# Performance work log

Measured on AMD Instinct MI355X. Metric: run time of the kernel, lower is better.

The kernel has to match this reference:

```python
import jax, jax.numpy as jnp
import numpy as np
import math

B, S, D, H = 2, 2048, 768, 12
HD = D // H


def setup_inputs() -> dict:
    key = jax.random.key(0)
    ks = jax.random.split(key, 9)
    scale = 1.0 / math.sqrt(D)
    x = jax.random.normal(ks[0], (B, S, D), dtype=jnp.float32)
    # causal mask: True where attention is allowed (query i attends to key j<=i)
    mask = jnp.tril(jnp.ones((S, S), dtype=bool))[None, None]  # [1,1,S,S]
    wq = jax.random.normal(ks[1], (D, D), dtype=jnp.float32) * scale
    bq = jnp.zeros((D,), dtype=jnp.float32)
    wk = jax.random.normal(ks[2], (D, D), dtype=jnp.float32) * scale
    bk = jnp.zeros((D,), dtype=jnp.float32)
    wv = jax.random.normal(ks[3], (D, D), dtype=jnp.float32) * scale
    bv = jnp.zeros((D,), dtype=jnp.float32)
    wo = jax.random.normal(ks[4], (D, D), dtype=jnp.float32) * scale
    bo = jnp.zeros((D,), dtype=jnp.float32)
    return {"x": x, "mask": mask, "wq": wq, "bq": bq, "wk": wk, "bk": bk,
            "wv": wv, "bv": bv, "wo": wo, "bo": bo}


def reference(x, mask, wq, bq, wk, bk, wv, bv, wo, bo):
    b, s, d = x.shape
    # projections (flax Linear: y = x @ kernel + bias)
    q = (x @ wq + bq).reshape(b, s, H, HD).transpose(0, 2, 1, 3)  # [b,h,s,hd]
    k = (x @ wk + bk).reshape(b, s, H, HD).transpose(0, 2, 1, 3)
    v = (x @ wv + bv).reshape(b, s, H, HD).transpose(0, 2, 1, 3)
    scores = jnp.einsum('bhqd,bhkd->bhqk', q, k) / math.sqrt(HD)  # [b,h,s,s]
    scores = jnp.where(mask, scores, -jnp.inf)
    attn = jax.nn.softmax(scores, axis=-1)
    out = jnp.einsum('bhqk,bhkd->bhqd', attn, v)  # [b,h,s,hd]
    out = out.transpose(0, 2, 1, 3).reshape(b, s, d)
    return out @ wo + bo
```

## Files before the change

kernel.cpp:

```cpp
#include <hip/hip_runtime.h>
#include <math.h>

#define BATCH 2
#define SEQ   2048
#define DMODEL 768
#define NHEAD 12
#define HDIM  64

typedef unsigned short u16;
typedef __attribute__((ext_vector_type(8))) short bf16x8;
typedef __attribute__((ext_vector_type(4))) float f32x4;
typedef __attribute__((ext_vector_type(8))) unsigned short us8;
typedef __attribute__((ext_vector_type(4))) unsigned short us4;

__device__ __forceinline__ u16 f2bf(float f) {
    union { float f; unsigned u; } v; v.f = f;
    unsigned u = v.u;
    u += 0x7fff + ((u >> 16) & 1);
    return (u16)(u >> 16);
}

__device__ __forceinline__ u16 f2bf_trunc(float f) {
    union { float f; unsigned u; } v; v.f = f;
    return (u16)(v.u >> 16);
}

__device__ __forceinline__ void g2l16(const void* g, void* l) {
    __builtin_amdgcn_global_load_lds(
        (const __attribute__((address_space(1))) unsigned int*)g,
        (__attribute__((address_space(3))) unsigned int*)(unsigned int)(unsigned long long)(uintptr_t)l,
        16, 0, 0);
}

__device__ __forceinline__ void stage_rows(const u16* g, u16* lds, int nrows,
                                           int tid) {
    const int row = tid >> 2, col = (tid & 3) * 8;
    g2l16(g + (size_t)row * DMODEL + col, lds + tid * 8);
    if (nrows == 128) {
        g2l16(g + (size_t)(row + 64) * DMODEL + col, lds + 2048 + tid * 8);
    } else if (nrows == 96) {
        if (tid < 128)
            g2l16(g + (size_t)(row + 64) * DMODEL + col, lds + 2048 + tid * 8);
    }
}

__global__ __launch_bounds__(256) void prep(const float* __restrict__ x,
                                            const float* __restrict__ w0,
                                            const float* __restrict__ w1,
                                            const float* __restrict__ w2,
                                            const float* __restrict__ w3,
                                            u16* __restrict__ xb,
                                            u16* __restrict__ Wt_all) {
    __shared__ float t[32][33];
    const int bid = blockIdx.x;
    if (bid < 3072) {
        int i = bid * 256 + threadIdx.x;
        float4 v = ((const float4*)x)[i];
        us4 o;
        o.x = f2bf(v.x); o.y = f2bf(v.y); o.z = f2bf(v.z); o.w = f2bf(v.w);
        *(us4*)&xb[(size_t)i * 4] = o;
    } else {
        const int wid = bid - 3072;
        const int z  = wid / 576;
        const int rr = wid % 576;
        const int by = rr / 24, bx = rr % 24;
        const float* W = z == 0 ? w0 : z == 1 ? w1 : z == 2 ? w2 : w3;
        u16* Wt = Wt_all + (size_t)z * DMODEL * DMODEL;

        int tx = threadIdx.x & 31, ty = threadIdx.x >> 5;
        int xg = bx * 32 + tx;
        #pragma unroll
        for (int j = 0; j < 32; j += 8)
            t[ty + j][tx] = W[(size_t)(by * 32 + ty + j) * DMODEL + xg];
        __syncthreads();
        int x2 = by * 32 + tx;
        #pragma unroll
        for (int j = 0; j < 32; j += 8)
            Wt[(size_t)(bx * 32 + ty + j) * DMODEL + x2] = f2bf(t[tx][ty + j]);
    }
}

__global__ __launch_bounds__(256) void gemm_qkv(
    const u16* __restrict__ xb, const u16* __restrict__ WtQK,
    const u16* __restrict__ WtV,
    const float* __restrict__ bq, const float* __restrict__ bk,
    const float* __restrict__ bv,
    u16* __restrict__ QK, u16* __restrict__ Vt) {

    __shared__ __align__(16) u16 As[128 * 32];
    __shared__ __align__(16) u16 Bs[128 * 32];

    const int tid  = threadIdx.x;
    const int lane = tid & 63;
    const int w    = tid >> 6;
    const int quad = lane >> 4, l16 = lane & 15;
    const int wm   = w >> 1, wn = w & 1;
    const int b    = blockIdx.x;

    if (b < 512) {
        const int m0 = (b >> 4) * 128;
        const int n0 = (b & 15) * 96;
        f32x4 acc[4][3] = {};
        for (int k0 = 0; k0 < DMODEL; k0 += 32) {
            stage_rows(xb   + (size_t)m0 * DMODEL + k0, As, 128, tid);
            stage_rows(WtQK + (size_t)n0 * DMODEL + k0, Bs,  96, tid);
            __syncthreads();
            bf16x8 af[4], bfr[3];
            #pragma unroll
            for (int i = 0; i < 4; ++i)
                af[i] = *(const bf16x8*)&As[(wm * 64 + i * 16 + l16) * 32 + quad * 8];
            #pragma unroll
            for (int j = 0; j < 3; ++j)
                bfr[j] = *(const bf16x8*)&Bs[(wn * 48 + j * 16 + l16) * 32 + quad * 8];
            #pragma unroll
            for (int i = 0; i < 4; ++i)
                #pragma unroll
                for (int j = 0; j < 3; ++j)
                    acc[i][j] = __builtin_amdgcn_mfma_f32_16x16x32_bf16(af[i], bfr[j], acc[i][j], 0, 0, 0);
            __syncthreads();
        }
        const size_t n_elem = (size_t)BATCH * SEQ * DMODEL;
        #pragma unroll
        for (int j = 0; j < 3; ++j) {
            const int n     = n0 + wn * 48 + j * 16 + l16;
            const int which = n / 768;
            const int nn    = n - which * 768;
            const float bias  = (which == 0 ? bq : bk)[nn];
            const float scale = (which == 0) ? 0.125f : 1.0f;
            const int h = nn >> 6, hd = nn & 63;
            u16* outw = QK + (size_t)which * n_elem;
            #pragma unroll
            for (int i = 0; i < 4; ++i) {
                const int mbase = m0 + wm * 64 + i * 16 + quad * 4;
                #pragma unroll
                for (int r = 0; r < 4; ++r) {
                    const int m  = mbase + r;
                    const int b_ = m >> 11, s_ = m & 2047;
                    outw[(size_t)((b_ * NHEAD + h) * SEQ + s_) * HDIM + hd] =
                        f2bf((acc[i][j][r] + bias) * scale);
                }
            }
        }
    } else {
        const int vj = b - 512;
        const int m0 = (vj & 7) * 96;
        const int n0 = (vj >> 3) * 128;
        f32x4 acc[3][4] = {};
        for (int k0 = 0; k0 < DMODEL; k0 += 32) {
            stage_rows(WtV + (size_t)m0 * DMODEL + k0, As,  96, tid);
            stage_rows(xb  + (size_t)n0 * DMODEL + k0, Bs, 128, tid);
            __syncthreads();
            bf16x8 af[3], bfr[4];
            #pragma unroll
            for (int i = 0; i < 3; ++i)
                af[i] = *(const bf16x8*)&As[(wm * 48 + i * 16 + l16) * 32 + quad * 8];
            #pragma unroll
            for (int j = 0; j < 4; ++j)
                bfr[j] = *(const bf16x8*)&Bs[(wn * 64 + j * 16 + l16) * 32 + quad * 8];
            #pragma unroll
            for (int i = 0; i < 3; ++i)
                #pragma unroll
                for (int j = 0; j < 4; ++j)
                    acc[i][j] = __builtin_amdgcn_mfma_f32_16x16x32_bf16(af[i], bfr[j], acc[i][j], 0, 0, 0);
            __syncthreads();
        }
        #pragma unroll
        for (int i = 0; i < 3; ++i) {
            const int rbase = m0 + wm * 48 + i * 16 + quad * 4;
            #pragma unroll
            for (int r = 0; r < 4; ++r) {
                const int row_g = rbase + r;
                const float bias = bv[row_g];
                const int h = row_g >> 6, hd = row_g & 63;
                #pragma unroll
                for (int j = 0; j < 4; ++j) {
                    const int col_g = n0 + wn * 64 + j * 16 + l16;
                    const int b_ = col_g >> 11, s_ = col_g & 2047;
                    Vt[(size_t)((b_ * NHEAD + h) * HDIM + hd) * SEQ + s_] =
                        f2bf(acc[i][j][r] + bias);
                }
            }
        }
    }
}

__global__ __launch_bounds__(256) void gemm_out(
    const u16* __restrict__ Ag, const u16* __restrict__ Bt,
    const float* __restrict__ bo, float* __restrict__ out) {

    __shared__ __align__(16) u16 As[64 * 32];
    __shared__ __align__(16) u16 Bs[64 * 32];

    const int tid  = threadIdx.x;
    const int lane = tid & 63;
    const int w    = tid >> 6;
    const int quad = lane >> 4, l16 = lane & 15;
    const int wm   = w >> 1, wn = w & 1;
    const int m0 = blockIdx.x * 64, n0 = blockIdx.y * 64;

    const int rowA = tid >> 2;
    const int kch  = (tid & 3) * 8;

    f32x4 acc[2][2] = {};

    for (int k0 = 0; k0 < DMODEL; k0 += 32) {
        g2l16(Ag + (size_t)(m0 + rowA) * DMODEL + k0 + kch, As + tid * 8);
        g2l16(Bt + (size_t)(n0 + rowA) * DMODEL + k0 + kch, Bs + tid * 8);
        __syncthreads();

        bf16x8 af[2], bfr[2];
        #pragma unroll
        for (int i = 0; i < 2; ++i)
            af[i] = *(const bf16x8*)&As[(wm * 32 + i * 16 + l16) * 32 + quad * 8];
        #pragma unroll
        for (int j = 0; j < 2; ++j)
            bfr[j] = *(const bf16x8*)&Bs[(wn * 32 + j * 16 + l16) * 32 + quad * 8];
        #pragma unroll
        for (int i = 0; i < 2; ++i)
            #pragma unroll
            for (int j = 0; j < 2; ++j)
                acc[i][j] = __builtin_amdgcn_mfma_f32_16x16x32_bf16(af[i], bfr[j], acc[i][j], 0, 0, 0);
        __syncthreads();
    }

    #pragma unroll
    for (int i = 0; i < 2; ++i) {
        const int mbase = m0 + wm * 32 + i * 16 + quad * 4;
        #pragma unroll
        for (int r = 0; r < 4; ++r) {
            const int m = mbase + r;
            #pragma unroll
            for (int j = 0; j < 2; ++j) {
                const int n = n0 + wn * 32 + j * 16 + l16;
                out[(size_t)m * DMODEL + n] = acc[i][j][r] + bo[n];
            }
        }
    }
}

__global__ __launch_bounds__(256) void flash_attn_mfma(
    const u16* __restrict__ Q, const u16* __restrict__ K,
    const u16* __restrict__ Vt, u16* __restrict__ A) {

    __shared__ __align__(16) u16 Kl[2][64 * 64];
    __shared__ __align__(16) u16 Vl[2][64 * 64];
    __shared__ __align__(16) u16 Pl[4][16 * 72];

    const int tid  = threadIdx.x;
    const int lane = tid & 63;
    const int w    = tid >> 6;
    const int quad = lane >> 4;
    const int l16  = lane & 15;

    const int lin = blockIdx.x;
    const int cc_ = lin & 255, rk = lin >> 8;
    const int sid = (rk << 8) + ((rk & 1) ? (255 - cc_) : cc_);
    const int j   = sid / 24;
    const int bh  = sid - j * 24;
    const int tc  = j + 1;

    const size_t base = (size_t)bh * SEQ * HDIM;
    const u16* Qg = Q + base;
    const u16* Kg = K + base;
    const u16* Vg = Vt + base;

    const int wrow0 = j * 64 + w * 16;
    const int qrow  = wrow0 + quad * 4;

    bf16x8 qf0 = *(const bf16x8*)&Qg[(size_t)(wrow0 + l16) * 64 + quad * 8];
    bf16x8 qf1 = *(const bf16x8*)&Qg[(size_t)(wrow0 + l16) * 64 + quad * 8 + 32];

    f32x4 o[4] = {};
    float l_acc[4] = {0.f, 0.f, 0.f, 0.f};

    const int pwbase = 2 * quad + (l16 >> 3);
    const int prd0   = (quad + 2 * (l16 >> 2)) & 7;
    u16* Pw = Pl[w];
    const u16* pr0 = &Pw[l16 * 72 + prd0 * 8];
    const u16* pr1 = &Pw[l16 * 72 + (prd0 ^ 4) * 8];

    auto STAGE = [&](int t, int b) {
        const int j0 = t * 64;
        #pragma unroll
        for (int h = 0; h < 2; ++h) {
            const int ch = tid + h * 256;
            const int r  = ch >> 3;
            const int lc = (ch & 7) ^ (r & 7);
            g2l16(Kg + (size_t)(j0 + r) * 64 + lc * 8, &Kl[b][ch * 8]);
            g2l16(Vg + (size_t)r * SEQ + j0 + lc * 8,  &Vl[b][ch * 8]);
        }
    };

    STAGE(0, 0);
    __syncthreads();

    int cur = 0;
    for (int t = 0; t < tc; ++t) {
        if (t + 1 < tc) STAGE(t + 1, cur ^ 1);

        const int j0 = t * 64;
        const u16* Kc = Kl[cur];
        const u16* Vc = Vl[cur];

        f32x4 s[4];
        #pragma unroll
        for (int c4 = 0; c4 < 4; ++c4) {
            const int krow = c4 * 16 + l16;
            const int pc = (quad ^ (krow & 7)) * 8;
            bf16x8 kf0 = *(const bf16x8*)&Kc[krow * 64 + pc];
            bf16x8 kf1 = *(const bf16x8*)&Kc[krow * 64 + (pc ^ 32)];
            f32x4 a2 = {};
            a2 = __builtin_amdgcn_mfma_f32_16x16x32_bf16(qf0, kf0, a2, 0, 0, 0);
            a2 = __builtin_amdgcn_mfma_f32_16x16x32_bf16(qf1, kf1, a2, 0, 0, 0);
            s[c4] = a2;
        }

        if (t == tc - 1) {
            #pragma unroll
            for (int c4 = 0; c4 < 4; ++c4) {
                const int jg = j0 + c4 * 16 + l16;
                #pragma unroll
                for (int r = 0; r < 4; ++r)
                    if (jg > qrow + r) s[c4][r] = -INFINITY;
            }
        }

        #pragma unroll
        for (int c4 = 0; c4 < 4; ++c4)
            #pragma unroll
            for (int r = 0; r < 4; ++r)
                s[c4][r] = __expf(s[c4][r]);
        #pragma unroll
        for (int r = 0; r < 4; ++r)
            l_acc[r] += (s[0][r] + s[1][r]) + (s[2][r] + s[3][r]);

        #pragma unroll
        for (int c4 = 0; c4 < 4; ++c4) {
            const int pc = ((2 * c4 + pwbase) & 7) * 8 + (l16 & 7);
            #pragma unroll
            for (int r = 0; r < 4; ++r)
                Pw[(quad * 4 + r) * 72 + pc] = f2bf_trunc(s[c4][r]);
        }
        bf16x8 pf0 = *(const bf16x8*)pr0;
        bf16x8 pf1 = *(const bf16x8*)pr1;

        #pragma unroll
        for (int c2 = 0; c2 < 4; ++c2) {
            const int vrow = c2 * 16 + l16;
            const int vc = (quad ^ (vrow & 7)) * 8;
            bf16x8 vf0 = *(const bf16x8*)&Vc[vrow * 64 + vc];
            bf16x8 vf1 = *(const bf16x8*)&Vc[vrow * 64 + (vc ^ 32)];
            o[c2] = __builtin_amdgcn_mfma_f32_16x16x32_bf16(pf0, vf0, o[c2], 0, 0, 0);
            o[c2] = __builtin_amdgcn_mfma_f32_16x16x32_bf16(pf1, vf1, o[c2], 0, 0, 0);
        }

        __syncthreads();
        cur ^= 1;
    }

    #pragma unroll
    for (int off = 1; off < 16; off <<= 1)
        #pragma unroll
        for (int r = 0; r < 4; ++r)
            l_acc[r] += __shfl_xor(l_acc[r], off);

    const int b = bh / NHEAD, h = bh % NHEAD;
    #pragma unroll
    for (int r = 0; r < 4; ++r) {
        float inv = 1.0f / l_acc[r];
        int sg = qrow + r;
        u16* dst = A + ((size_t)(b * SEQ + sg)) * DMODEL + h * HDIM;
        #pragma unroll
        for (int c2 = 0; c2 < 4; ++c2)
            dst[c2 * 16 + l16] = f2bf(o[c2][r] * inv);
    }
}

extern "C" void kernel_launch(void* const* d_in, const int* in_sizes, int n_in,
                              void* d_out, int out_size, void* d_ws, size_t ws_size,
                              hipStream_t stream) {
    const float* x  = (const float*)d_in[0];
    const float* wq = (const float*)d_in[2];
    const float* bq = (const float*)d_in[3];
    const float* wk = (const float*)d_in[4];
    const float* bk = (const float*)d_in[5];
    const float* wv = (const float*)d_in[6];
    const float* bv = (const float*)d_in[7];
    const float* wo = (const float*)d_in[8];
    const float* bo = (const float*)d_in[9];
    float* out = (float*)d_out;

    const size_t n_elem = (size_t)BATCH * SEQ * DMODEL;
    const size_t w_elem = (size_t)DMODEL * DMODEL;

    u16* xb     = (u16*)d_ws;
    u16* Wt_all = xb + n_elem;
    u16* Qw     = Wt_all + 4 * w_elem;
    u16* Vtw    = Qw + 2 * n_elem;
    u16* Aw     = Vtw + n_elem;

    dim3 blk(256);

    prep<<<dim3(3072 + 2304), blk, 0, stream>>>(x, wq, wk, wv, wo, xb, Wt_all);

    gemm_qkv<<<dim3(768), blk, 0, stream>>>(xb, Wt_all, Wt_all + 2 * w_elem,
                                            bq, bk, bv, Qw, Vtw);

    flash_attn_mfma<<<dim3(768), blk, 0, stream>>>(Qw, Qw + n_elem, Vtw, Aw);

    gemm_out<<<dim3(64, 12), blk, 0, stream>>>(Aw, Wt_all + 3 * w_elem, bo, out);
}
```

Baseline: 166.8 us.

## Triple-buffer flash-attention K/V staging with vmcnt waits, exp2 softmax, and reordered scheduling

Moves the attention K/V staging from a double buffer to a triple buffer with two tiles in flight. Per-iteration __syncthreads is replaced by an explicit s_waitcnt vmcnt plus a single barrier, and staging pointers are precomputed and advanced incrementally. The Q scale now folds in log2(e) so the softmax can use the hardware exp2 instruction. MFMA sections are wrapped in s_setprio, and block order becomes longest-first (reverse linear), replacing the snake pattern. The extra buffer adds LDS and may lower occupancy, and the hand-written vmcnt counts must match the actual number of outstanding loads.

```diff
diff --git a/kernel.cpp b/kernel.cpp
--- a/kernel.cpp
+++ b/kernel.cpp
@@ -23,6 +23,14 @@
 __device__ __forceinline__ u16 f2bf_trunc(float f) {
     union { float f; unsigned u; } v; v.f = f;
     return (u16)(v.u >> 16);
+}
+
+__device__ __forceinline__ float fexp2(float x) {
+#if __has_builtin(__builtin_amdgcn_exp2f)
+    return __builtin_amdgcn_exp2f(x);
+#else
+    return exp2f(x);
+#endif
 }
 
 __device__ __forceinline__ void g2l16(const void* g, void* l) {
@@ -126,7 +134,7 @@
             const int which = n / 768;
             const int nn    = n - which * 768;
             const float bias  = (which == 0 ? bq : bk)[nn];
-            const float scale = (which == 0) ? 0.125f : 1.0f;
+            const float scale = (which == 0) ? 0.18033688011112043f : 1.0f;
             const int h = nn >> 6, hd = nn & 63;
             u16* outw = QK + (size_t)which * n_elem;
             #pragma unroll
@@ -242,8 +250,8 @@
     const u16* __restrict__ Q, const u16* __restrict__ K,
     const u16* __restrict__ Vt, u16* __restrict__ A) {
 
-    __shared__ __align__(16) u16 Kl[2][64 * 64];
-    __shared__ __align__(16) u16 Vl[2][64 * 64];
+    __shared__ __align__(16) u16 Kl[3][64 * 64];
+    __shared__ __align__(16) u16 Vl[3][64 * 64];
     __shared__ __align__(16) u16 Pl[4][16 * 72];
 
     const int tid  = threadIdx.x;
@@ -252,9 +260,7 @@
     const int quad = lane >> 4;
     const int l16  = lane & 15;
 
-    const int lin = blockIdx.x;
-    const int cc_ = lin & 255, rk = lin >> 8;
-    const int sid = (rk << 8) + ((rk & 1) ? (255 - cc_) : cc_);
+    const int sid = 767 - (int)blockIdx.x;
     const int j   = sid / 24;
     const int bh  = sid - j * 24;
     const int tc  = j + 1;
@@ -279,30 +285,39 @@
     const u16* pr0 = &Pw[l16 * 72 + prd0 * 8];
     const u16* pr1 = &Pw[l16 * 72 + (prd0 ^ 4) * 8];
 
-    auto STAGE = [&](int t, int b) {
-        const int j0 = t * 64;
-        #pragma unroll
-        for (int h = 0; h < 2; ++h) {
-            const int ch = tid + h * 256;
-            const int r  = ch >> 3;
-            const int lc = (ch & 7) ^ (r & 7);
-            g2l16(Kg + (size_t)(j0 + r) * 64 + lc * 8, &Kl[b][ch * 8]);
-            g2l16(Vg + (size_t)r * SEQ + j0 + lc * 8,  &Vl[b][ch * 8]);
-        }
+    const int ch0 = tid, ch1 = tid + 256;
+    const int r0 = ch0 >> 3, lc0 = (ch0 & 7) ^ (r0 & 7);
+    const int r1 = ch1 >> 3, lc1 = (ch1 & 7) ^ (r1 & 7);
+    const u16* kp0 = Kg + (size_t)r0 * 64 + lc0 * 8;
+    const u16* kp1 = Kg + (size_t)r1 * 64 + lc1 * 8;
+    const u16* vp0 = Vg + (size_t)r0 * SEQ + lc0 * 8;
+    const u16* vp1 = Vg + (size_t)r1 * SEQ + lc1 * 8;
+
+    auto STAGE = [&](int buf) {
+        g2l16(kp0, &Kl[buf][ch0 * 8]);
+        g2l16(kp1, &Kl[buf][ch1 * 8]);
+        g2l16(vp0, &Vl[buf][ch0 * 8]);
+        g2l16(vp1, &Vl[buf][ch1 * 8]);
+        kp0 += 64 * 64; kp1 += 64 * 64;
+        vp0 += 64;      vp1 += 64;
     };
 
-    STAGE(0, 0);
-    __syncthreads();
-
-    int cur = 0;
+    STAGE(0);
+    if (tc > 1) STAGE(1);
+
+    int cur = 0, nb = 2;
     for (int t = 0; t < tc; ++t) {
-        if (t + 1 < tc) STAGE(t + 1, cur ^ 1);
+        if (t + 1 < tc) asm volatile("s_waitcnt vmcnt(4)" ::: "memory");
+        else            asm volatile("s_waitcnt vmcnt(0)" ::: "memory");
+        __builtin_amdgcn_s_barrier();
+        if (t + 2 < tc) { STAGE(nb); nb = (nb == 2) ? 0 : nb + 1; }
 
         const int j0 = t * 64;
         const u16* Kc = Kl[cur];
         const u16* Vc = Vl[cur];
 
         f32x4 s[4];
+        __builtin_amdgcn_s_setprio(1);
         #pragma unroll
         for (int c4 = 0; c4 < 4; ++c4) {
             const int krow = c4 * 16 + l16;
@@ -314,6 +329,7 @@
             a2 = __builtin_amdgcn_mfma_f32_16x16x32_bf16(qf1, kf1, a2, 0, 0, 0);
             s[c4] = a2;
         }
+        __builtin_amdgcn_s_setprio(0);
 
         if (t == tc - 1) {
             #pragma unroll
@@ -329,7 +345,7 @@
         for (int c4 = 0; c4 < 4; ++c4)
             #pragma unroll
             for (int r = 0; r < 4; ++r)
-                s[c4][r] = __expf(s[c4][r]);
+                s[c4][r] = fexp2(s[c4][r]);
         #pragma unroll
         for (int r = 0; r < 4; ++r)
             l_acc[r] += (s[0][r] + s[1][r]) + (s[2][r] + s[3][r]);
@@ -344,6 +360,7 @@
         bf16x8 pf0 = *(const bf16x8*)pr0;
         bf16x8 pf1 = *(const bf16x8*)pr1;
 
+        __builtin_amdgcn_s_setprio(1);
         #pragma unroll
         for (int c2 = 0; c2 < 4; ++c2) {
             const int vrow = c2 * 16 + l16;
@@ -353,9 +370,9 @@
             o[c2] = __builtin_amdgcn_mfma_f32_16x16x32_bf16(pf0, vf0, o[c2], 0, 0, 0);
             o[c2] = __builtin_amdgcn_mfma_f32_16x16x32_bf16(pf1, vf1, o[c2], 0, 0, 0);
         }
-
-        __syncthreads();
-        cur ^= 1;
+        __builtin_amdgcn_s_setprio(0);
+
+        cur = (cur == 2) ? 0 : cur + 1;
     }
 
     #pragma unroll
```

Result: faster. 162.3 us (-2.7%).
